# Optimization experiments

Hardware: AMD Instinct MI355X
Metric: run time of the kernel (lower is better)

## Reference

```python
import jax, jax.numpy as jnp
import numpy as np

INV_SQRT2 = 0.7071067811865476
N_ATOMS, N_EDGES, KMAX, N_SPH = 5000, 100000, 10, 7
E, A, T, R, C, B = 512, 128, 64, 16, 16, 64  # edge, atom, trip, rbf, cbf-interm, bilinear


def _act(x):
    # GemNet ScaledSiLU: silu(x) / 0.6
    return jax.nn.silu(x) * (1.0 / 0.6)


def _residual(x, W0, W1):
    y = _act(_act(x @ W0) @ W1)
    return (x + y) * INV_SQRT2


def setup_inputs() -> dict:
    key = jax.random.key(0)
    ks = jax.random.split(key, 24)

    def w(k, shape):
        return jax.random.normal(k, shape, jnp.float32) / np.float32(np.sqrt(shape[-2]))

    nT = N_EDGES * KMAX  # 1M triplets; (id3_reduce_ca, Kidx3) pairs unique
    inp = {
        "h": jax.random.normal(ks[0], (N_ATOMS, A), jnp.float32),
        "m": jax.random.normal(ks[1], (N_EDGES, E), jnp.float32),
        "rbf3": jax.random.normal(ks[2], (N_EDGES, R), jnp.float32),
        "cbf_W1": jax.random.normal(ks[3], (N_EDGES, C, N_SPH), jnp.float32),
        "cbf_sph": jax.random.normal(ks[4], (N_EDGES, KMAX, N_SPH), jnp.float32),
        "rbf_h": jax.random.normal(ks[5], (N_EDGES, R), jnp.float32),
        "W_dense_ca": w(ks[6], (E, E)),
        "W_ba": w(ks[7], (E, E)),
        "W_rbf3": w(ks[8], (R, E)),
        "W_down": w(ks[9], (E, T)),
        "W_bil": jax.random.normal(ks[10], (T, C, B), jnp.float32) / np.float32(np.sqrt(T * C)),
        "W_up_ca": w(ks[11], (B, E)),
        "W_up_ac": w(ks[12], (B, E)),
        "W_res_before": w(ks[13], (1, 2, E, E)),
        "W_res_after": w(ks[14], (2, 2, E, E)),
        "W_rbf_h": w(ks[15], (R, E)),
        "W_atom_dense": w(ks[16], (E, A)),
        "W_atom_res": w(ks[17], (3, 2, A, A)),
        "W_concat": w(ks[18], (2 * A + E, E)),
        "W_res_m": w(ks[19], (1, 2, E, E)),
        "Kidx3": jnp.tile(jnp.arange(KMAX, dtype=jnp.int32), N_EDGES),
        "id_swap": jax.random.permutation(ks[20], N_EDGES).astype(jnp.int32),
        "id3_expand_ba": jax.random.randint(ks[21], (nT,), 0, N_EDGES, jnp.int32),
        "id3_reduce_ca": jnp.repeat(jnp.arange(N_EDGES, dtype=jnp.int32), KMAX),
        "id_c": jax.random.randint(ks[22], (N_EDGES,), 0, N_ATOMS, jnp.int32),
        "id_a": jax.random.randint(ks[23], (N_EDGES,), 0, N_ATOMS, jnp.int32),
    }
    return inp


def reference(h, m, rbf3, cbf_W1, cbf_sph, rbf_h,
              W_dense_ca, W_ba, W_rbf3, W_down, W_bil, W_up_ca, W_up_ac,
              W_res_before, W_res_after, W_rbf_h, W_atom_dense, W_atom_res,
              W_concat, W_res_m,
              Kidx3, id_swap, id3_expand_ba, id3_reduce_ca, id_c, id_a):
    nEdges = m.shape[0]
    Kmax = cbf_sph.shape[1]

    # ---- skip branch ----
    x_ca_skip = _act(m @ W_dense_ca)

    # ---- TripletInteraction ----
    x_ba = _act(m @ W_ba)
    x_ba = x_ba * (rbf3 @ W_rbf3)            # hadamard with rbf MLP (scale=1)
    x_ba = _act(x_ba @ W_down)               # (nEdges, T)
    x_ba = x_ba[id3_expand_ba]               # gather -> (nTriplets, T)
    # EfficientInteractionBilinear: scatter triplets into (nEdges, Kmax, T)
    m2 = jnp.zeros((nEdges, Kmax, x_ba.shape[-1]), m.dtype).at[id3_reduce_ca, Kidx3].set(x_ba)
    sum_k = jnp.einsum('eks,eki->esi', cbf_sph, m2)   # (E, S, T)
    rW = jnp.einsum('ejs,esi->eji', cbf_W1, sum_k)    # (E, C, T)
    x = jnp.einsum('eji,ijo->eo', rW, W_bil)          # (E, B); scale=1
    x_ca = _act(x @ W_up_ca)
    x_ac = _act(x @ W_up_ac)[id_swap]
    x3 = (x_ca + x_ac) * INV_SQRT2

    x = (x_ca_skip + x3) * INV_SQRT2
    for i in range(W_res_before.shape[0]):
        x = _residual(x, W_res_before[i, 0], W_res_before[i, 1])
    m_new = (m + x) * INV_SQRT2
    for i in range(W_res_after.shape[0]):
        m_new = _residual(m_new, W_res_after[i, 0], W_res_after[i, 1])

    # ---- AtomUpdateBlock ----
    xm = m_new * (rbf_h @ W_rbf_h)
    x2 = jax.ops.segment_sum(xm, id_a, num_segments=h.shape[0])  # scale=1
    xa = _act(x2 @ W_atom_dense)
    for i in range(W_atom_res.shape[0]):
        xa = _residual(xa, W_atom_res[i, 0], W_atom_res[i, 1])
    h_new = (h + xa) * INV_SQRT2

    # ---- EdgeEmbedding (concat) ----
    mc = _act(jnp.concatenate([h_new[id_c], h_new[id_a], m_new], axis=-1) @ W_concat)
    for i in range(W_res_m.shape[0]):
        mc = _residual(mc, W_res_m[i, 0], W_res_m[i, 1])
    m_out = (m_new + mc) * INV_SQRT2
    return h_new, m_out
```

## Files before the change

### kernel.cpp

```cpp
#include <hip/hip_runtime.h>
#include <cstdint>

#define NE 100000
#define NA 5000
#define DE 512
#define DAH 128
#define DT 64
#define NS 7
#define KM 10
#define DR 16
#define INV2 0.70710678118654752440f

typedef __attribute__((ext_vector_type(8))) short short8;
typedef __attribute__((ext_vector_type(4))) float floatx4;
typedef __attribute__((ext_vector_type(4))) unsigned short ushort4v;
typedef unsigned short u16;
typedef unsigned int u32;

__device__ __forceinline__ float bf2f(u16 u){ u32 x = ((u32)u)<<16; return __builtin_bit_cast(float, x); }
__device__ __forceinline__ u16 f2bf(float f){ u32 u = __builtin_bit_cast(u32, f); u += 0x7FFFu + ((u>>16)&1u); return (u16)(u>>16); }
__device__ __forceinline__ float actf(float x){
  float e = __expf(-x);
  float s = __builtin_amdgcn_rcpf(1.0f + e);
  return x * s * (1.0f/0.6f);
}

__device__ __forceinline__ void gl16(const u16* g, u16* l){
  __builtin_amdgcn_global_load_lds(
      (const __attribute__((address_space(1))) u32*)g,
      (__attribute__((address_space(3))) u32*)l, 16, 0, 0);
}

struct TEntry { const float* s; u16* d; int K; int N; };
struct TArgs { TEntry e[24]; };
__global__ __launch_bounds__(256) void prep_k(TArgs a){
  TEntry en = a.e[blockIdx.y];
  long total = (long)en.K * en.N;
  for (long i = (long)blockIdx.x*256 + threadIdx.x; i < total; i += (long)gridDim.x*256){
    long n = i / en.K, k = i - n*en.K;
    en.d[i] = f2bf(en.s[k*(long)en.N + n]);
  }
}

__global__ __launch_bounds__(256) void mb_k(const float* __restrict__ src, u16* __restrict__ dst){
  const long i = ((long)blockIdx.x*256 + threadIdx.x)*8;
  if (i >= (long)NE*DE) return;
  floatx4 a0 = *(const floatx4*)(src+i), a1 = *(const floatx4*)(src+i+4);
  short8 v;
#pragma unroll
  for (int j=0;j<4;j++){ v[j]=(short)f2bf(a0[j]); v[j+4]=(short)f2bf(a1[j]); }
  *(short8*)(dst+i) = v;
}

struct GemmArgs {
  const void* A; const u16* Bt; void* Out;
  const u16* Had; const void* Res1; const void* Res2;
  const float* Hn; const u16* Mn; const int* idc; const int* ida;
  int M, N, K;
};

template<int BM,int BN,int WGM,int WGN,int AMODE,int EP,int OUTF,int R1F,int R2F>
__global__ __launch_bounds__(256)
void gemm_k(GemmArgs g){
  __shared__ __align__(16) u16 As[BM*32];
  __shared__ __align__(16) u16 Bs[BN*32];
  constexpr int WM = BM/(WGM*16), WN = BN/(WGN*16);
  const int t = threadIdx.x;
  const long row0 = (long)blockIdx.x*BM;
  const int col0 = blockIdx.y*BN;
  const int wave = t>>6, lane = t&63;
  const int wm = wave/WGN, wn = wave%WGN;
  const int lrow = lane&15, q = lane>>4;
  const int sr4 = lane>>2, ch = lane&3;
  floatx4 acc[WM][WN];
#pragma unroll
  for (int a=0;a<WM;a++)
#pragma unroll
    for (int b=0;b<WN;b++) acc[a][b] = (floatx4){0.f,0.f,0.f,0.f};

  for (int k0=0; k0<g.K; k0+=32){
    if (k0) __syncthreads();
#pragma unroll
    for (int i=0;i<BN/64;i++){
      const int slot = wave*(BN/64) + i;
      const int rb = slot*16 + sr4;
      const int sw = ch ^ ((rb + (rb>>2)) & 3);
      gl16(g.Bt + (long)(col0+rb)*g.K + k0 + (sw<<3), &Bs[slot*512]);
    }
    if constexpr (AMODE==0){
#pragma unroll
      for (int i=0;i<BM/64;i++){
        const int slot = wave*(BM/64) + i;
        const int ra = slot*16 + sr4;
        const int sw = ch ^ ((ra + (ra>>2)) & 3);
        gl16((const u16*)g.A + (row0+ra)*(long)g.K + k0 + (sw<<3), &As[slot*512]);
      }
    } else {
#pragma unroll
      for (int c = t; c < BM*4; c += 256){
        const int r = c>>2, kch = c&3, kc = kch*8;
        const long gr = row0 + r; const int gk = k0 + kc;
        short8 v = {0,0,0,0,0,0,0,0};
        if (gr < g.M && gk < g.K){
          if constexpr (AMODE==1){
            const float* ap = (const float*)g.A + gr*(long)g.K + gk;
            floatx4 a0 = *(const floatx4*)ap, a1 = *(const floatx4*)(ap+4);
#pragma unroll
            for (int j=0;j<4;j++){ v[j]=(short)f2bf(a0[j]); v[j+4]=(short)f2bf(a1[j]); }
          } else {
            if (gk < DAH){
              const float* hp = g.Hn + (long)g.idc[gr]*DAH + gk;
              floatx4 a0 = *(const floatx4*)hp, a1 = *(const floatx4*)(hp+4);
#pragma unroll
              for (int j=0;j<4;j++){ v[j]=(short)f2bf(a0[j]); v[j+4]=(short)f2bf(a1[j]); }
            } else if (gk < 2*DAH){
              const float* hp = g.Hn + (long)g.ida[gr]*DAH + (gk-DAH);
              floatx4 a0 = *(const floatx4*)hp, a1 = *(const floatx4*)(hp+4);
#pragma unroll
              for (int j=0;j<4;j++){ v[j]=(short)f2bf(a0[j]); v[j+4]=(short)f2bf(a1[j]); }
            } else {
              v = *(const short8*)(g.Mn + gr*(long)DE + (gk-2*DAH));
            }
          }
        }
        const int dch = kch ^ ((r + (r>>2)) & 3);
        *(short8*)&As[r*32 + dch*8] = v;
      }
    }
    __syncthreads();
    short8 af[WM], bfr[WN];
#pragma unroll
    for (int mi=0;mi<WM;mi++){
      const int R = wm*WM*16 + mi*16 + lrow;
      af[mi] = *(const short8*)&As[R*32 + ((q ^ ((R + (R>>2))&3))<<3)];
    }
#pragma unroll
    for (int ni=0;ni<WN;ni++){
      const int R = wn*WN*16 + ni*16 + lrow;
      bfr[ni] = *(const short8*)&Bs[R*32 + ((q ^ ((R + (R>>2))&3))<<3)];
    }
#pragma unroll
    for (int mi=0;mi<WM;mi++)
#pragma unroll
      for (int ni=0;ni<WN;ni++)
        acc[mi][ni] = __builtin_amdgcn_mfma_f32_16x16x32_bf16(af[mi], bfr[ni], acc[mi][ni], 0,0,0);
  }
#pragma unroll
  for (int mi=0;mi<WM;mi++){
#pragma unroll
    for (int ni=0;ni<WN;ni++){
      const int gcol = col0 + wn*WN*16 + ni*16 + lrow;
      if (gcol < g.N){
#pragma unroll
        for (int r=0;r<4;r++){
          const long grow = row0 + wm*WM*16 + mi*16 + q*4 + r;
          if (grow < g.M){
            float v = acc[mi][ni][r];
            const long oi = grow*(long)g.N + gcol;
            if constexpr (EP==1) v = actf(v);
            if constexpr (EP==2) v = actf(v) * bf2f(g.Had[oi]);
            if constexpr (EP==3){
              float r1 = R1F ? ((const float*)g.Res1)[oi] : bf2f(((const u16*)g.Res1)[oi]);
              v = (r1 + actf(v)) * INV2;
            }
            if constexpr (EP==4){
              float r1 = R1F ? ((const float*)g.Res1)[oi] : bf2f(((const u16*)g.Res1)[oi]);
              float r2 = R2F ? ((const float*)g.Res2)[oi] : bf2f(((const u16*)g.Res2)[oi]);
              v = (r2 + (r1 + actf(v))*INV2) * INV2;
            }
            if constexpr (OUTF) ((float*)g.Out)[oi] = v;
            else ((u16*)g.Out)[oi] = f2bf(v);
          }
        }
      }
    }
  }
}

__global__ __launch_bounds__(256) void trip_k(const u16* __restrict__ xba2,
    const float* __restrict__ cbf_sph, const float* __restrict__ cbf_w1,
    const int* __restrict__ id3e, u16* __restrict__ rw){
  const int e = blockIdx.x*4 + (threadIdx.x>>6);
  if (e >= NE) return;
  const int lane = threadIdx.x & 63;
  float m2[KM];
#pragma unroll
  for (int k=0;k<KM;k++){
    const int idx = id3e[e*KM + k];
    m2[k] = bf2f(xba2[(long)idx*DT + lane]);
  }
  const float* sph = cbf_sph + (long)e*KM*NS;
  float sk[NS];
#pragma unroll
  for (int s=0;s<NS;s++){
    float acc = 0.f;
#pragma unroll
    for (int k=0;k<KM;k++) acc += sph[k*NS+s]*m2[k];
    sk[s] = acc;
  }
  const float* w1 = cbf_w1 + (long)e*16*NS;
  short8 v0, v1;
#pragma unroll
  for (int j=0;j<16;j++){
    float acc = 0.f;
#pragma unroll
    for (int s=0;s<NS;s++) acc += w1[j*NS+s]*sk[s];
    if (j<8) v0[j] = (short)f2bf(acc); else v1[j-8] = (short)f2bf(acc);
  }
  u16* dst = rw + (long)e*1024 + lane*16;
  *(short8*)dst = v0;
  *(short8*)(dst+8) = v1;
}

__global__ __launch_bounds__(256) void comb_k(const u16* __restrict__ S, u16* __restrict__ C,
    const u16* __restrict__ D, const int* __restrict__ swp){
  const long i = ((long)blockIdx.x*256 + threadIdx.x)*8;
  if (i >= (long)NE*DE) return;
  const long r = i >> 9; const int c = (int)(i & 511);
  const int sr = swp[r];
  short8 s8 = *(const short8*)(S+i);
  short8 c8 = *(const short8*)(C+i);
  short8 d8 = *(const short8*)(D + (long)sr*DE + c);
  short8 o;
#pragma unroll
  for (int j=0;j<8;j++)
    o[j] = (short)f2bf((bf2f((u16)s8[j]) + (bf2f((u16)c8[j]) + bf2f((u16)d8[j]))*INV2)*INV2);
  *(short8*)(C+i) = o;
}

__global__ __launch_bounds__(256) void hist_k(const int* __restrict__ ida, int* __restrict__ cnt){
  const int e = blockIdx.x*256 + threadIdx.x;
  if (e < NE) atomicAdd(&cnt[ida[e]], 1);
}

__global__ __launch_bounds__(256) void scan_k(const int* __restrict__ cnt,
    int* __restrict__ off, int* __restrict__ cur){
  __shared__ int s[256];
  const int t = threadIdx.x;
  const int base = t*20;
  int loc[20]; int sum = 0;
#pragma unroll
  for (int j=0;j<20;j++){
    int v = (base+j < NA) ? cnt[base+j] : 0;
    loc[j] = sum; sum += v;
  }
  s[t] = sum;
  __syncthreads();
  for (int d=1; d<256; d<<=1){
    int v = (t>=d) ? s[t-d] : 0;
    __syncthreads();
    s[t] += v;
    __syncthreads();
  }
  const int excl = (t==0) ? 0 : s[t-1];
#pragma unroll
  for (int j=0;j<20;j++){
    if (base+j < NA){ off[base+j] = excl + loc[j]; cur[base+j] = excl + loc[j]; }
  }
  if (t==255) off[NA] = s[255];
}

__global__ __launch_bounds__(256) void fill_k(const int* __restrict__ ida,
    int* __restrict__ cur, int* __restrict__ csr){
  const int e = blockIdx.x*256 + threadIdx.x;
  if (e >= NE) return;
  const int a = ida[e];
  const int pos = atomicAdd(&cur[a], 1);
  csr[pos] = e;
}

__global__ __launch_bounds__(256) void gath_k(const u16* __restrict__ mn,
    const float* __restrict__ rbfh, const u16* __restrict__ wt ,
    const int* __restrict__ off, const int* __restrict__ csr, float* __restrict__ x2){
  const int a = blockIdx.x;
  const int t = threadIdx.x;
  float w0[16], w1[16];
  const u16* wp = wt + (t*2)*16;
#pragma unroll
  for (int k=0;k<16;k++){ w0[k] = bf2f(wp[k]); w1[k] = bf2f(wp[16+k]); }
  const int beg = off[a], end = off[a+1];
  float acc0 = 0.f, acc1 = 0.f;
  for (int i=beg; i<end; ++i){
    const int e = csr[i];
    const float* rp = rbfh + (long)e*DR;
    floatx4 r0 = *(const floatx4*)rp;
    floatx4 r1 = *(const floatx4*)(rp+4);
    floatx4 r2 = *(const floatx4*)(rp+8);
    floatx4 r3 = *(const floatx4*)(rp+12);
    const u32 mv = *(const u32*)(mn + ((long)e<<9) + t*2);
    float rb0 = 0.f, rb1 = 0.f;
#pragma unroll
    for (int j=0;j<4;j++){
      rb0 += r0[j]*w0[j]   + r1[j]*w0[4+j] + r2[j]*w0[8+j] + r3[j]*w0[12+j];
      rb1 += r0[j]*w1[j]   + r1[j]*w1[4+j] + r2[j]*w1[8+j] + r3[j]*w1[12+j];
    }
    acc0 += bf2f((u16)mv)       * rb0;
    acc1 += bf2f((u16)(mv>>16)) * rb1;
  }
  float* dst = x2 + ((long)a<<9) + t*2;
  dst[0] = acc0; dst[1] = acc1;
}

extern "C" void kernel_launch(void* const* d_in, const int* in_sizes, int n_in,
                              void* d_out, int out_size, void* d_ws, size_t ws_size,
                              hipStream_t stream){
  (void)in_sizes; (void)n_in; (void)out_size;
  const float* h    = (const float*)d_in[0];
  const float* m    = (const float*)d_in[1];
  const float* rbf3 = (const float*)d_in[2];
  const float* cbfW1= (const float*)d_in[3];
  const float* cbfS = (const float*)d_in[4];
  const float* rbfh = (const float*)d_in[5];
  const float* W_dense=(const float*)d_in[6];
  const float* W_ba  =(const float*)d_in[7];
  const float* W_rbf3=(const float*)d_in[8];
  const float* W_down=(const float*)d_in[9];
  const float* W_bil =(const float*)d_in[10];
  const float* W_upca=(const float*)d_in[11];
  const float* W_upac=(const float*)d_in[12];
  const float* W_rb  =(const float*)d_in[13];
  const float* W_ra  =(const float*)d_in[14];
  const float* W_rbfh=(const float*)d_in[15];
  const float* W_ad  =(const float*)d_in[16];
  const float* W_ar  =(const float*)d_in[17];
  const float* W_cat =(const float*)d_in[18];
  const float* W_rm  =(const float*)d_in[19];
  const int* id_swap =(const int*)d_in[21];
  const int* id3e    =(const int*)d_in[22];
  const int* id_c    =(const int*)d_in[24];
  const int* id_a    =(const int*)d_in[25];

  char* p = (char*)d_ws;
  auto alloc = [&](size_t b)->char*{ char* r=p; p += (b+255)&~(size_t)255; return r; };

  const size_t SLOT = (size_t)NE*DE*2;
  u16* BIG = (u16*)alloc(4*SLOT);
  u16* B0 = BIG;
  u16* B1 = BIG + SLOT/2;
  u16* B2 = BIG + 2*(SLOT/2);
  u16* B3 = BIG + 3*(SLOT/2);
  u16* rw = B0;

  u16* wt_dense=(u16*)alloc(512*512*2);
  u16* wt_ba   =(u16*)alloc(512*512*2);
  u16* wt_rbf3 =(u16*)alloc(16*512*2);
  u16* wt_down =(u16*)alloc(512*64*2);
  u16* wt_bil  =(u16*)alloc(1024*64*2);
  u16* wt_upca =(u16*)alloc(64*512*2);
  u16* wt_upac =(u16*)alloc(64*512*2);
  u16* wt_rb0  =(u16*)alloc(512*512*2);
  u16* wt_rb1  =(u16*)alloc(512*512*2);
  u16* wt_ra[4]; for (int i=0;i<4;i++) wt_ra[i]=(u16*)alloc(512*512*2);
  u16* wt_rbfh =(u16*)alloc(16*512*2);
  u16* wt_ad   =(u16*)alloc(512*128*2);
  u16* wt_ar[6]; for (int i=0;i<6;i++) wt_ar[i]=(u16*)alloc(128*128*2);
  u16* wt_cat  =(u16*)alloc(768*512*2);
  u16* wt_rm0  =(u16*)alloc(512*512*2);
  u16* wt_rm1  =(u16*)alloc(512*512*2);
  u16* xba2 = (u16*)alloc((size_t)NE*DT*2);
  u16* xbil = (u16*)alloc((size_t)NE*DT*2);
  float* x2 = (float*)alloc((size_t)NA*DE*4);
  float* xa = (float*)alloc((size_t)NA*DAH*4);
  float* yb = (float*)alloc((size_t)NA*DAH*4);
  int* csr_cnt = (int*)alloc((size_t)NA*4);
  int* csr_off = (int*)alloc((size_t)(NA+1)*4);
  int* csr_cur = (int*)alloc((size_t)NA*4);
  int* csr_edg = (int*)alloc((size_t)NE*4);
  float* out_h = (float*)d_out;
  float* out_m = (float*)d_out + (size_t)NA*DAH;

  size_t used = (size_t)(p - (char*)d_ws);
  const bool use_mbf = ws_size > used + SLOT + (1u<<20);
  u16* mbf = nullptr;
  if (use_mbf) mbf = (u16*)alloc(SLOT + (1u<<17));

  TArgs ta;
  int ti=0;
  auto te=[&](const float* s, u16* d, int K, int N){ ta.e[ti++] = {s,d,K,N}; };
  te(W_dense,wt_dense,512,512); te(W_ba,wt_ba,512,512); te(W_rbf3,wt_rbf3,16,512);
  te(W_down,wt_down,512,64);   te(W_bil,wt_bil,1024,64);
  te(W_upca,wt_upca,64,512);   te(W_upac,wt_upac,64,512);
  te(W_rb,wt_rb0,512,512);     te(W_rb+262144,wt_rb1,512,512);
  for (int i=0;i<4;i++) te(W_ra+(size_t)i*262144, wt_ra[i],512,512);
  te(W_rbfh,wt_rbfh,16,512);   te(W_ad,wt_ad,512,128);
  for (int i=0;i<6;i++) te(W_ar+(size_t)i*16384, wt_ar[i],128,128);
  te(W_cat,wt_cat,768,512);    te(W_rm,wt_rm0,512,512); te(W_rm+262144,wt_rm1,512,512);
  prep_k<<<dim3(128,24),256,0,stream>>>(ta);

  if (use_mbf) mb_k<<<NE*DE/8/256,256,0,stream>>>(m, mbf);

  hipMemsetAsync(csr_cnt, 0, (size_t)NA*4, stream);
  hist_k<<<(NE+255)/256,256,0,stream>>>(id_a, csr_cnt);
  scan_k<<<1,256,0,stream>>>(csr_cnt, csr_off, csr_cur);
  fill_k<<<(NE+255)/256,256,0,stream>>>(id_a, csr_cur, csr_edg);

  const dim3 GE128(782,4);
  const dim3 GE64 (782,1);
  const dim3 GAT  (40,2);

  GemmArgs ga;
  ga = {}; ga.A=rbf3; ga.Bt=wt_rbf3; ga.Out=B0; ga.M=NE; ga.N=DE; ga.K=DR;
  gemm_k<128,128,2,2,1,0,0,0,0><<<GE128,256,0,stream>>>(ga);
  if (use_mbf){
    ga = {}; ga.A=mbf; ga.Bt=wt_dense; ga.Out=B2; ga.M=NE; ga.N=DE; ga.K=DE;
    gemm_k<128,128,2,2,0,1,0,0,0><<<GE128,256,0,stream>>>(ga);
  } else {
    ga = {}; ga.A=m; ga.Bt=wt_dense; ga.Out=B2; ga.M=NE; ga.N=DE; ga.K=DE;
    gemm_k<128,128,2,2,1,1,0,0,0><<<GE128,256,0,stream>>>(ga);
  }
  if (use_mbf){
    ga = {}; ga.A=mbf; ga.Bt=wt_ba; ga.Out=B1; ga.Had=B0; ga.M=NE; ga.N=DE; ga.K=DE;
    gemm_k<128,128,2,2,0,2,0,0,0><<<GE128,256,0,stream>>>(ga);
  } else {
    ga = {}; ga.A=m; ga.Bt=wt_ba; ga.Out=B1; ga.Had=B0; ga.M=NE; ga.N=DE; ga.K=DE;
    gemm_k<128,128,2,2,1,2,0,0,0><<<GE128,256,0,stream>>>(ga);
  }
  ga = {}; ga.A=B1; ga.Bt=wt_down; ga.Out=xba2; ga.M=NE; ga.N=DT; ga.K=DE;
  gemm_k<128,64,4,1,0,1,0,0,0><<<GE64,256,0,stream>>>(ga);
  trip_k<<<NE/4,256,0,stream>>>(xba2, cbfS, cbfW1, id3e, rw);
  ga = {}; ga.A=rw; ga.Bt=wt_bil; ga.Out=xbil; ga.M=NE; ga.N=DT; ga.K=1024;
  gemm_k<128,64,4,1,0,0,0,0,0><<<GE64,256,0,stream>>>(ga);
  ga = {}; ga.A=xbil; ga.Bt=wt_upca; ga.Out=B3; ga.M=NE; ga.N=DE; ga.K=DT;
  gemm_k<128,128,2,2,0,1,0,0,0><<<GE128,256,0,stream>>>(ga);
  ga = {}; ga.A=xbil; ga.Bt=wt_upac; ga.Out=B0; ga.M=NE; ga.N=DE; ga.K=DT;
  gemm_k<128,128,2,2,0,1,0,0,0><<<GE128,256,0,stream>>>(ga);
  comb_k<<<NE*DE/8/256,256,0,stream>>>(B2, B3, B0, id_swap);
  ga = {}; ga.A=B3; ga.Bt=wt_rb0; ga.Out=B1; ga.M=NE; ga.N=DE; ga.K=DE;
  gemm_k<128,128,2,2,0,1,0,0,0><<<GE128,256,0,stream>>>(ga);
  if (use_mbf){
    ga = {}; ga.A=B1; ga.Bt=wt_rb1; ga.Out=B2; ga.Res1=B3; ga.Res2=mbf; ga.M=NE; ga.N=DE; ga.K=DE;
    gemm_k<128,128,2,2,0,4,0,0,0><<<GE128,256,0,stream>>>(ga);
  } else {
    ga = {}; ga.A=B1; ga.Bt=wt_rb1; ga.Out=B2; ga.Res1=B3; ga.Res2=m; ga.M=NE; ga.N=DE; ga.K=DE;
    gemm_k<128,128,2,2,0,4,0,0,1><<<GE128,256,0,stream>>>(ga);
  }
  ga = {}; ga.A=B2; ga.Bt=wt_ra[0]; ga.Out=B1; ga.M=NE; ga.N=DE; ga.K=DE;
  gemm_k<128,128,2,2,0,1,0,0,0><<<GE128,256,0,stream>>>(ga);
  ga = {}; ga.A=B1; ga.Bt=wt_ra[1]; ga.Out=B0; ga.Res1=B2; ga.M=NE; ga.N=DE; ga.K=DE;
  gemm_k<128,128,2,2,0,3,0,0,0><<<GE128,256,0,stream>>>(ga);
  ga = {}; ga.A=B0; ga.Bt=wt_ra[2]; ga.Out=B1; ga.M=NE; ga.N=DE; ga.K=DE;
  gemm_k<128,128,2,2,0,1,0,0,0><<<GE128,256,0,stream>>>(ga);
  ga = {}; ga.A=B1; ga.Bt=wt_ra[3]; ga.Out=B2; ga.Res1=B0; ga.M=NE; ga.N=DE; ga.K=DE;
  gemm_k<128,128,2,2,0,3,0,0,0><<<GE128,256,0,stream>>>(ga);
  gath_k<<<NA,256,0,stream>>>(B2, rbfh, wt_rbfh, csr_off, csr_edg, x2);
  ga = {}; ga.A=x2; ga.Bt=wt_ad; ga.Out=xa; ga.M=NA; ga.N=DAH; ga.K=DE;
  gemm_k<128,64,4,1,1,1,1,0,0><<<GAT,256,0,stream>>>(ga);
  for (int i=0;i<2;i++){
    ga = {}; ga.A=xa; ga.Bt=wt_ar[2*i]; ga.Out=yb; ga.M=NA; ga.N=DAH; ga.K=DAH;
    gemm_k<128,64,4,1,1,1,1,0,0><<<GAT,256,0,stream>>>(ga);
    ga = {}; ga.A=yb; ga.Bt=wt_ar[2*i+1]; ga.Out=xa; ga.Res1=xa; ga.M=NA; ga.N=DAH; ga.K=DAH;
    gemm_k<128,64,4,1,1,3,1,1,0><<<GAT,256,0,stream>>>(ga);
  }
  ga = {}; ga.A=xa; ga.Bt=wt_ar[4]; ga.Out=yb; ga.M=NA; ga.N=DAH; ga.K=DAH;
  gemm_k<128,64,4,1,1,1,1,0,0><<<GAT,256,0,stream>>>(ga);
  ga = {}; ga.A=yb; ga.Bt=wt_ar[5]; ga.Out=out_h; ga.Res1=xa; ga.Res2=h; ga.M=NA; ga.N=DAH; ga.K=DAH;
  gemm_k<128,64,4,1,1,4,1,1,1><<<GAT,256,0,stream>>>(ga);
  ga = {}; ga.Bt=wt_cat; ga.Out=B1; ga.Hn=out_h; ga.Mn=B2; ga.idc=id_c; ga.ida=id_a;
  ga.M=NE; ga.N=DE; ga.K=2*DAH+DE;
  gemm_k<128,128,2,2,2,1,0,0,0><<<GE128,256,0,stream>>>(ga);
  ga = {}; ga.A=B1; ga.Bt=wt_rm0; ga.Out=B0; ga.M=NE; ga.N=DE; ga.K=DE;
  gemm_k<128,128,2,2,0,1,0,0,0><<<GE128,256,0,stream>>>(ga);
  ga = {}; ga.A=B0; ga.Bt=wt_rm1; ga.Out=out_m; ga.Res1=B1; ga.Res2=B2; ga.M=NE; ga.N=DE; ga.K=DE;
  gemm_k<128,128,2,2,0,4,1,0,0><<<GE128,256,0,stream>>>(ga);
}
```

Before: 2.753 ms.

## Triple-buffer GEMM LDS tiles with async prefetch and fragment-ordered layout

Changes the GEMM main loop from a single-buffered load-sync-compute pattern to a three-stage ring of LDS buffers. Tiles two steps ahead are prefetched while the current one feeds the MFMAs, with waits controlled by explicit vmcnt counts. The LDS layout is also switched from a swizzled row-major layout to one stored in MFMA fragment order, so each lane reads one contiguous short8. This costs triple the LDS per block, which can lower occupancy, and relies on hand-placed waitcnt and barriers being correct.

```diff
diff --git a/kernel.cpp b/kernel.cpp
--- a/kernel.cpp
+++ b/kernel.cpp
@@ -62,38 +62,30 @@
 template<int BM,int BN,int WGM,int WGN,int AMODE,int EP,int OUTF,int R1F,int R2F>
 __global__ __launch_bounds__(256)
 void gemm_k(GemmArgs g){
-  __shared__ __align__(16) u16 As[BM*32];
-  __shared__ __align__(16) u16 Bs[BN*32];
+  __shared__ __align__(16) u16 As[3][BM*32];
+  __shared__ __align__(16) u16 Bs[3][BN*32];
   constexpr int WM = BM/(WGM*16), WN = BN/(WGN*16);
+  constexpr int KLD = BN/64 + (AMODE==0 ? BM/64 : 0);
   const int t = threadIdx.x;
   const long row0 = (long)blockIdx.x*BM;
   const int col0 = blockIdx.y*BN;
   const int wave = t>>6, lane = t&63;
   const int wm = wave/WGN, wn = wave%WGN;
   const int lrow = lane&15, q = lane>>4;
-  const int sr4 = lane>>2, ch = lane&3;
+  const int NT = (g.K+31)>>5;
   floatx4 acc[WM][WN];
 #pragma unroll
   for (int a=0;a<WM;a++)
 #pragma unroll
     for (int b=0;b<WN;b++) acc[a][b] = (floatx4){0.f,0.f,0.f,0.f};
 
-  for (int k0=0; k0<g.K; k0+=32){
-    if (k0) __syncthreads();
-#pragma unroll
-    for (int i=0;i<BN/64;i++){
-      const int slot = wave*(BN/64) + i;
-      const int rb = slot*16 + sr4;
-      const int sw = ch ^ ((rb + (rb>>2)) & 3);
-      gl16(g.Bt + (long)(col0+rb)*g.K + k0 + (sw<<3), &Bs[slot*512]);
-    }
+  auto stage = [&](int ti, int b){
+    const int k0 = ti<<5;
     if constexpr (AMODE==0){
 #pragma unroll
       for (int i=0;i<BM/64;i++){
-        const int slot = wave*(BM/64) + i;
-        const int ra = slot*16 + sr4;
-        const int sw = ch ^ ((ra + (ra>>2)) & 3);
-        gl16((const u16*)g.A + (row0+ra)*(long)g.K + k0 + (sw<<3), &As[slot*512]);
+        const int slot = wave*(BM/64)+i;
+        gl16((const u16*)g.A + (row0 + slot*16 + lrow)*(long)g.K + k0 + (q<<3), &As[b][slot*512]);
       }
     } else {
 #pragma unroll
@@ -123,27 +115,40 @@
             }
           }
         }
-        const int dch = kch ^ ((r + (r>>2)) & 3);
-        *(short8*)&As[r*32 + dch*8] = v;
+        *(short8*)&As[b][(r>>4)*512 + kch*128 + (r&15)*8] = v;
       }
     }
-    __syncthreads();
+#pragma unroll
+    for (int i=0;i<BN/64;i++){
+      const int slot = wave*(BN/64)+i;
+      gl16(g.Bt + (long)(col0 + slot*16 + lrow)*g.K + k0 + (q<<3), &Bs[b][slot*512]);
+    }
+  };
+
+  stage(0,0);
+  if (NT>1) stage(1,1);
+  int cb = 0;
+  for (int ti=0; ti<NT; ++ti){
+    if (ti+2<NT) stage(ti+2, cb==0?2:(cb-1));
+    if (ti+2<NT)      asm volatile("s_waitcnt vmcnt(%0)"::"i"(2*KLD):"memory");
+    else if (ti+1<NT) asm volatile("s_waitcnt vmcnt(%0)"::"i"(KLD):"memory");
+    else              asm volatile("s_waitcnt vmcnt(0)":::"memory");
+    if constexpr (AMODE!=0) asm volatile("s_waitcnt lgkmcnt(0)":::"memory");
+    __builtin_amdgcn_s_barrier();
+    __builtin_amdgcn_sched_barrier(0);
     short8 af[WM], bfr[WN];
 #pragma unroll
-    for (int mi=0;mi<WM;mi++){
-      const int R = wm*WM*16 + mi*16 + lrow;
-      af[mi] = *(const short8*)&As[R*32 + ((q ^ ((R + (R>>2))&3))<<3)];
-    }
-#pragma unroll
-    for (int ni=0;ni<WN;ni++){
-      const int R = wn*WN*16 + ni*16 + lrow;
-      bfr[ni] = *(const short8*)&Bs[R*32 + ((q ^ ((R + (R>>2))&3))<<3)];
-    }
+    for (int mi=0;mi<WM;mi++) af[mi]  = *(const short8*)&As[cb][(wm*WM+mi)*512 + lane*8];
+#pragma unroll
+    for (int ni=0;ni<WN;ni++) bfr[ni] = *(const short8*)&Bs[cb][(wn*WN+ni)*512 + lane*8];
 #pragma unroll
     for (int mi=0;mi<WM;mi++)
 #pragma unroll
       for (int ni=0;ni<WN;ni++)
         acc[mi][ni] = __builtin_amdgcn_mfma_f32_16x16x32_bf16(af[mi], bfr[ni], acc[mi][ni], 0,0,0);
+    __builtin_amdgcn_sched_barrier(0);
+    __builtin_amdgcn_s_barrier();
+    cb = (cb==2)?0:cb+1;
   }
 #pragma unroll
   for (int mi=0;mi<WM;mi++){
```

New measurement: 3.067 ms. +11.4%, slower.
